# Kernel tuning notes

Measured on AMD Instinct MI355X. Metric: run time of the kernel, lower is better.

Reference implementation:

```python
import jax, jax.numpy as jnp
import numpy as np

SCALE_FACTORS = (1, 2, 4)
N, T, F = 4096, 128, 128
MARKET = 64
MIX = sum(T // k for k in SCALE_FACTORS)  # 224


def hardswish(x):
    return x * jnp.clip(x + 3.0, 0.0, 6.0) * (1.0 / 6.0)


def layernorm2d(x, g, b, eps=1e-5):
    # LayerNorm with normalized_shape == last two dims (as in torch nn.LayerNorm((A, B)))
    mu = jnp.mean(x, axis=(-2, -1), keepdims=True)
    var = jnp.var(x, axis=(-2, -1), keepdims=True)
    return (x - mu) * jax.lax.rsqrt(var + eps) * g + b


def setup_inputs() -> dict:
    key = jax.random.key(0)
    ks = jax.random.split(key, 32)
    inp = {"x": jax.random.normal(ks[0], (N, T, F), jnp.float32)}
    i = 1
    for si, k in enumerate(SCALE_FACTORS):
        tk = T // k
        inp[f"cw{si}"] = jax.random.normal(ks[i], (F, F, k), jnp.float32) * 0.05; i += 1
        inp[f"cb{si}"] = jnp.zeros((F,), jnp.float32)
        inp[f"lg{si}"] = jnp.ones((tk, F), jnp.float32)
        inp[f"lb{si}"] = jnp.zeros((tk, F), jnp.float32)
        inp[f"L1_{si}"] = jax.random.normal(ks[i], (tk, tk), jnp.float32) * 0.01; i += 1
        inp[f"L2_{si}"] = jax.random.normal(ks[i], (tk, tk), jnp.float32) * 0.01; i += 1
    inp["fc_w"] = jax.random.normal(ks[i], (1, F), jnp.float32) * 0.05; i += 1
    inp["fc_b"] = jnp.zeros((1,), jnp.float32)
    inp["sm_lg"] = jnp.ones((N, MIX), jnp.float32)
    inp["sm_lb"] = jnp.zeros((N, MIX), jnp.float32)
    inp["M1"] = jax.random.normal(ks[i], (MARKET, N), jnp.float32); i += 1
    inp["M2"] = jax.random.normal(ks[i], (N, MARKET), jnp.float32); i += 1
    inp["sm_fc_w"] = jax.random.normal(ks[i], (1, 2 * MIX), jnp.float32) * 0.02; i += 1
    inp["sm_fc_b"] = jnp.zeros((1,), jnp.float32)
    return inp


def _forward(x, cw0, cb0, lg0, lb0, L1_0, L2_0,
             cw1, cb1, lg1, lb1, L1_1, L2_1,
             cw2, cb2, lg2, lb2, L1_2, L2_2,
             fc_w, fc_b, sm_lg, sm_lb, M1, M2, sm_fc_w, sm_fc_b):
    n, t, f = x.shape
    per_scale = ((cw0, cb0, lg0, lb0, L1_0, L2_0),
                 (cw1, cb1, lg1, lb1, L1_1, L2_1),
                 (cw2, cb2, lg2, lb2, L1_2, L2_2))
    parts = []
    for k, (cw, cb, lg, lb, L1, L2) in zip(SCALE_FACTORS, per_scale):
        tk = t // k
        # Conv1d(kernel=k, stride=k) == blockwise contraction over non-overlapping windows
        xr = x.transpose(0, 2, 1).reshape(n, f, tk, k)          # (n, F_in, tk, k)
        xt = jnp.einsum('nitk,oik->nto', xr, cw) + cb            # (n, tk, F)
        # TimeMixing: ragged prefix loop == single lower-triangular matmul over time
        mask = jnp.tril(jnp.ones((tk, tk), x.dtype))
        h = layernorm2d(xt, lg, lb)
        u = hardswish(jnp.einsum('ts,nsf->ntf', L1 * mask, h))
        v = jnp.einsum('ts,nsf->ntf', L2 * mask, u)
        xt = xt + v
        parts.append(xt @ fc_w[0] + fc_b[0])                     # (n, tk)
    h = jnp.concatenate(parts, axis=1)                           # (n, MIX)
    # StockMixing
    hn = layernorm2d(h, sm_lg, sm_lb)
    z = M2 @ hardswish(M1 @ hn)                                  # (n, MIX)
    out = jnp.concatenate([h, h + z], axis=1)                    # (n, 2*MIX)
    return out @ sm_fc_w[0][:, None] + sm_fc_b                   # (n, 1)


def reference(x, cw0, cb0, lg0, lb0, L1_0, L2_0,
              cw1, cb1, lg1, lb1, L1_1, L2_1,
              cw2, cb2, lg2, lb2, L1_2, L2_2,
              fc_w, fc_b, sm_lg, sm_lb, M1, M2, sm_fc_w, sm_fc_b):
    return _forward(x, cw0, cb0, lg0, lb0, L1_0, L2_0,
                    cw1, cb1, lg1, lb1, L1_1, L2_1,
                    cw2, cb2, lg2, lb2, L1_2, L2_2,
                    fc_w, fc_b, sm_lg, sm_lb, M1, M2, sm_fc_w, sm_fc_b)
```

## Files before the change

### kernel.cpp

```cpp
#include <hip/hip_runtime.h>
#include <stdint.h>

typedef __attribute__((ext_vector_type(8))) short short8;
typedef __attribute__((ext_vector_type(4))) float f32x4;
typedef __attribute__((ext_vector_type(4))) unsigned short us4;

__device__ __forceinline__ unsigned short f2bf(float f) {
  union { float f; unsigned int i; } v; v.f = f;
  unsigned int r = (v.i + 0x7FFFu + ((v.i >> 16) & 1u)) >> 16;
  return (unsigned short)r;
}
__device__ __forceinline__ float hswish(float x) {
  float t = fminf(fmaxf(x + 3.f, 0.f), 6.f);
  return x * t * (1.f / 6.f);
}

__global__ void prep_kernel(const float* __restrict__ cw0,
                            const float* __restrict__ cw1,
                            const float* __restrict__ cw2,
                            unsigned short* __restrict__ cwLT0,
                            unsigned short* __restrict__ cwLT1,
                            unsigned short* __restrict__ cwLT2) {
  int idx = blockIdx.x * 256 + threadIdx.x;
  if (idx < 16384) {
    cwLT0[idx] = f2bf(cw0[idx]);
  } else if (idx < 16384 + 32768) {
    int t = idx - 16384;
    int o = t >> 8, m = t & 255;
    int j = m >> 7, i = m & 127;
    cwLT1[o * 256 + m] = f2bf(cw1[(o * 128 + i) * 2 + j]);
  } else if (idx < 114688) {
    int t = idx - 49152;
    int o = t >> 9, m = t & 511;
    int j = m >> 7, i = m & 127;
    cwLT2[o * 512 + m] = f2bf(cw2[(o * 128 + i) * 4 + j]);
  }
}

template <int S>
__launch_bounds__(256, 2)
__global__ void s1_kernel(const float* __restrict__ x,
                          const float* __restrict__ cb,
                          const float* __restrict__ lg,
                          const float* __restrict__ lb,
                          const float* __restrict__ L1,
                          const float* __restrict__ L2,
                          const float* __restrict__ fc_w,
                          const float* __restrict__ fc_b,
                          const unsigned short* __restrict__ cwLT,
                          float* __restrict__ h_out) {
  constexpr int K   = 128 << S;
  constexpr int TK  = 128 >> S;
  constexpr int OFF = (S == 0) ? 0 : (S == 1 ? 128 : 192);
  constexpr int nT  = (S == 0) ? 2 : 1;
  constexpr int nO  = (S == 2) ? 4 : 8;
  constexpr int CW  = (TK >= 64) ? 64 : TK;
  constexpr int NCC = K / 64;
  constexpr int NTC = TK / CW;
  constexpr int HTP = TK + 8;
  constexpr int LP  = CW + 8;
  constexpr int R1E = (HTP > 72 ? HTP : 72) * 128;

  extern __shared__ char smem[];
  unsigned short* R0 = (unsigned short*)smem;
  unsigned short* R1 = (unsigned short*)(smem + TK * 72 * 2);
  float* scratch = (float*)(smem + TK * 72 * 2 + R1E * 2);

  const int tid  = threadIdx.x;
  const int wave = tid >> 6;
  const int lane = tid & 63;
  const int quad = lane >> 4;
  const int l16  = lane & 15;
  const int n    = blockIdx.x;
  const float* xn = x + (size_t)n * (128 * 128);

  const int Tbase = (S == 0) ? wave * 2 : ((S == 1) ? wave : (wave & 1));
  const int Obase = (S == 2) ? ((wave >> 1) * 4) : 0;

  if (tid < 128) scratch[tid] = fc_w[tid];
  if (tid < TK) scratch[128 + tid] = 0.f;

  f32x4 acc[nT][nO];
#pragma unroll
  for (int tt = 0; tt < nT; ++tt)
#pragma unroll
    for (int oo = 0; oo < nO; ++oo)
      acc[tt][oo] = (f32x4){0.f, 0.f, 0.f, 0.f};

  for (int c = 0; c < NCC; ++c) {
    for (int i = tid; i < TK * 16; i += 256) {
      int t = i >> 4, c4 = (i & 15) * 4;
      const float4 v = *(const float4*)(xn + t * K + c * 64 + c4);
      us4 p; p[0] = f2bf(v.x); p[1] = f2bf(v.y); p[2] = f2bf(v.z); p[3] = f2bf(v.w);
      *(us4*)&R0[t * 72 + c4] = p;
    }
    for (int i = tid; i < 128 * 16; i += 256) {
      int o = i >> 4, c4 = (i & 15) * 4;
      *(us4*)&R1[o * 72 + c4] = *(const us4*)&cwLT[o * K + c * 64 + c4];
    }
    __syncthreads();
#pragma unroll
    for (int ks = 0; ks < 2; ++ks) {
      short8 a[nT];
#pragma unroll
      for (int tt = 0; tt < nT; ++tt)
        a[tt] = *(const short8*)&R0[((Tbase + tt) * 16 + l16) * 72 + ks * 32 + quad * 8];
#pragma unroll
      for (int oo = 0; oo < nO; ++oo) {
        short8 b = *(const short8*)&R1[((Obase + oo) * 16 + l16) * 72 + ks * 32 + quad * 8];
#pragma unroll
        for (int tt = 0; tt < nT; ++tt)
          acc[tt][oo] = __builtin_amdgcn_mfma_f32_16x16x32_bf16(a[tt], b, acc[tt][oo], 0, 0, 0);
      }
    }
    __syncthreads();
  }

  float sum = 0.f, ss = 0.f;
#pragma unroll
  for (int oo = 0; oo < nO; ++oo) {
    float cbv = cb[(Obase + oo) * 16 + l16];
#pragma unroll
    for (int tt = 0; tt < nT; ++tt)
#pragma unroll
      for (int r = 0; r < 4; ++r) {
        float v = acc[tt][oo][r] + cbv;
        acc[tt][oo][r] = v;
        sum += v; ss += v * v;
      }
  }
#pragma unroll
  for (int m = 32; m >= 1; m >>= 1) {
    sum += __shfl_xor(sum, m);
    ss  += __shfl_xor(ss, m);
  }
  if (lane == 0) { scratch[256 + wave * 2] = sum; scratch[257 + wave * 2] = ss; }
  __syncthreads();
  if (tid == 0) {
    float Sm = 0.f, Ssq = 0.f;
    for (int w = 0; w < 4; ++w) { Sm += scratch[256 + w * 2]; Ssq += scratch[257 + w * 2]; }
    float mu = Sm / (float)(TK * 128);
    float var = Ssq / (float)(TK * 128) - mu * mu;
    scratch[264] = mu;
    scratch[265] = rsqrtf(var + 1e-5f);
  }
  __syncthreads();
  const float mu = scratch[264], rsig = scratch[265];

  unsigned short* HT = R1;
#pragma unroll
  for (int tt = 0; tt < nT; ++tt)
#pragma unroll
    for (int oo = 0; oo < nO; ++oo) {
      int o = (Obase + oo) * 16 + l16;
#pragma unroll
      for (int r = 0; r < 4; ++r) {
        int t = (Tbase + tt) * 16 + quad * 4 + r;
        float hv = (acc[tt][oo][r] - mu) * rsig * lg[t * 128 + o] + lb[t * 128 + o];
        HT[o * HTP + t] = f2bf(hv);
      }
    }

  f32x4 uacc[nT][nO];
#pragma unroll
  for (int tt = 0; tt < nT; ++tt)
#pragma unroll
    for (int oo = 0; oo < nO; ++oo)
      uacc[tt][oo] = (f32x4){0.f, 0.f, 0.f, 0.f};

  for (int c = 0; c < NTC; ++c) {
    for (int i = tid; i < TK * (CW / 4); i += 256) {
      int t = i / (CW / 4), s4 = (i % (CW / 4)) * 4;
      int sg = c * CW + s4;
      const float4 v = *(const float4*)(L1 + t * TK + sg);
      us4 p;
      p[0] = (sg     <= t) ? f2bf(v.x) : (unsigned short)0;
      p[1] = (sg + 1 <= t) ? f2bf(v.y) : (unsigned short)0;
      p[2] = (sg + 2 <= t) ? f2bf(v.z) : (unsigned short)0;
      p[3] = (sg + 3 <= t) ? f2bf(v.w) : (unsigned short)0;
      *(us4*)&R0[t * LP + s4] = p;
    }
    __syncthreads();
#pragma unroll
    for (int ks = 0; ks < CW / 32; ++ks) {
      int k0 = c * CW + ks * 32;
      if (k0 <= (Tbase + nT - 1) * 16 + 15) {
        short8 a[nT];
#pragma unroll
        for (int tt = 0; tt < nT; ++tt)
          a[tt] = *(const short8*)&R0[((Tbase + tt) * 16 + l16) * LP + ks * 32 + quad * 8];
#pragma unroll
        for (int oo = 0; oo < nO; ++oo) {
          short8 b = *(const short8*)&HT[((Obase + oo) * 16 + l16) * HTP + k0 + quad * 8];
#pragma unroll
          for (int tt = 0; tt < nT; ++tt)
            if (k0 <= (Tbase + tt) * 16 + 15)
              uacc[tt][oo] = __builtin_amdgcn_mfma_f32_16x16x32_bf16(a[tt], b, uacc[tt][oo], 0, 0, 0);
        }
      }
      __syncthreads();
    }
  }

#pragma unroll
  for (int tt = 0; tt < nT; ++tt)
#pragma unroll
    for (int oo = 0; oo < nO; ++oo) {
      int f = (Obase + oo) * 16 + l16;
#pragma unroll
      for (int r = 0; r < 4; ++r) {
        int t = (Tbase + tt) * 16 + quad * 4 + r;
        float uv = hswish(uacc[tt][oo][r]);
        HT[f * HTP + t] = f2bf(uv);
      }
    }

  for (int c = 0; c < NTC; ++c) {
    for (int i = tid; i < TK * (CW / 4); i += 256) {
      int t = i / (CW / 4), s4 = (i % (CW / 4)) * 4;
      int sg = c * CW + s4;
      const float4 v = *(const float4*)(L2 + t * TK + sg);
      us4 p;
      p[0] = (sg     <= t) ? f2bf(v.x) : (unsigned short)0;
      p[1] = (sg + 1 <= t) ? f2bf(v.y) : (unsigned short)0;
      p[2] = (sg + 2 <= t) ? f2bf(v.z) : (unsigned short)0;
      p[3] = (sg + 3 <= t) ? f2bf(v.w) : (unsigned short)0;
      *(us4*)&R0[t * LP + s4] = p;
    }
    __syncthreads();
#pragma unroll
    for (int ks = 0; ks < CW / 32; ++ks) {
      int k0 = c * CW + ks * 32;
      if (k0 <= (Tbase + nT - 1) * 16 + 15) {
        short8 a[nT];
#pragma unroll
        for (int tt = 0; tt < nT; ++tt)
          a[tt] = *(const short8*)&R0[((Tbase + tt) * 16 + l16) * LP + ks * 32 + quad * 8];
#pragma unroll
        for (int oo = 0; oo < nO; ++oo) {
          short8 b = *(const short8*)&HT[((Obase + oo) * 16 + l16) * HTP + k0 + quad * 8];
#pragma unroll
          for (int tt = 0; tt < nT; ++tt)
            if (k0 <= (Tbase + tt) * 16 + 15)
              acc[tt][oo] = __builtin_amdgcn_mfma_f32_16x16x32_bf16(a[tt], b, acc[tt][oo], 0, 0, 0);
        }
      }
      __syncthreads();
    }
  }

  float* part = scratch + 128;
#pragma unroll
  for (int tt = 0; tt < nT; ++tt)
#pragma unroll
    for (int r = 0; r < 4; ++r) {
      float v = 0.f;
#pragma unroll
      for (int oo = 0; oo < nO; ++oo)
        v += acc[tt][oo][r] * scratch[(Obase + oo) * 16 + l16];
      v += __shfl_xor(v, 1); v += __shfl_xor(v, 2);
      v += __shfl_xor(v, 4); v += __shfl_xor(v, 8);
      if (l16 == 0) atomicAdd(&part[(Tbase + tt) * 16 + quad * 4 + r], v);
    }
  __syncthreads();
  if (tid < TK) h_out[(size_t)n * 224 + OFF + tid] = part[tid] + fc_b[0];
}

__global__ void stats_kernel(const float* __restrict__ h, float* __restrict__ stats) {
  int base = blockIdx.x * 4096;
  float s = 0.f, ss = 0.f;
  for (int j = 0; j < 16; ++j) {
    float v = h[base + j * 256 + threadIdx.x];
    s += v; ss += v * v;
  }
  int lane = threadIdx.x & 63, wave = threadIdx.x >> 6;
#pragma unroll
  for (int m = 32; m >= 1; m >>= 1) { s += __shfl_xor(s, m); ss += __shfl_xor(ss, m); }
  __shared__ float red[8];
  if (lane == 0) { red[wave * 2] = s; red[wave * 2 + 1] = ss; }
  __syncthreads();
  if (threadIdx.x == 0) {
    atomicAdd(&stats[0], red[0] + red[2] + red[4] + red[6]);
    atomicAdd(&stats[1], red[1] + red[3] + red[5] + red[7]);
  }
}

__global__ void mix1_kernel(const float* __restrict__ h,
                            const float* __restrict__ sm_lg,
                            const float* __restrict__ sm_lb,
                            const float* __restrict__ M1,
                            const float* __restrict__ stats,
                            float* __restrict__ A) {
  const int m = blockIdx.x;
  const int seg = blockIdx.y;
  const int r = threadIdx.x & 63;
  const int ch = threadIdx.x >> 6;
  const float inv = 1.f / 917504.f;
  float mu = stats[0] * inv;
  float var = stats[1] * inv - mu * mu;
  float rsig = rsqrtf(var + 1e-5f);
  float acc = 0.f;
  int n0 = seg * 1024 + ch * 256;
  for (int i = 0; i < 256; ++i) {
    int n = n0 + i;
    float hn = (h[n * 224 + m] - mu) * rsig * sm_lg[n * 224 + m] + sm_lb[n * 224 + m];
    acc += M1[r * 4096 + n] * hn;
  }
  __shared__ float red[256];
  red[threadIdx.x] = acc;
  __syncthreads();
  if (threadIdx.x < 64)
    atomicAdd(&A[threadIdx.x * 224 + m],
              red[threadIdx.x] + red[64 + threadIdx.x] + red[128 + threadIdx.x] + red[192 + threadIdx.x]);
}

__global__ void mix2_kernel(const float* __restrict__ A,
                            const float* __restrict__ sm_fc_w,
                            float* __restrict__ cvec) {
  int r = threadIdx.x & 63, ch = threadIdx.x >> 6;
  float acc = 0.f;
  for (int j = ch; j < 224; j += 4)
    acc += hswish(A[r * 224 + j]) * sm_fc_w[224 + j];
  __shared__ float red[256];
  red[threadIdx.x] = acc;
  __syncthreads();
  if (threadIdx.x < 64)
    cvec[threadIdx.x] = red[threadIdx.x] + red[64 + threadIdx.x] + red[128 + threadIdx.x] + red[192 + threadIdx.x];
}

__global__ void out_kernel(const float* __restrict__ h,
                           const float* __restrict__ M2,
                           const float* __restrict__ cvec,
                           const float* __restrict__ sm_fc_w,
                           const float* __restrict__ sm_fc_b,
                           float* __restrict__ out) {
  int wave = threadIdx.x >> 6, lane = threadIdx.x & 63;
  int n = blockIdx.x * 4 + wave;
  float acc = M2[n * 64 + lane] * cvec[lane];
  for (int j = lane; j < 224; j += 64)
    acc += h[n * 224 + j] * (sm_fc_w[j] + sm_fc_w[224 + j]);
#pragma unroll
  for (int m = 32; m >= 1; m >>= 1) acc += __shfl_xor(acc, m);
  if (lane == 0) out[n] = acc + sm_fc_b[0];
}

extern "C" void kernel_launch(void* const* d_in, const int* in_sizes, int n_in,
                              void* d_out, int out_size, void* d_ws, size_t ws_size,
                              hipStream_t stream) {
  const float* x      = (const float*)d_in[0];
  const float* cw0    = (const float*)d_in[1];
  const float* cb0    = (const float*)d_in[2];
  const float* lg0    = (const float*)d_in[3];
  const float* lb0    = (const float*)d_in[4];
  const float* L1_0   = (const float*)d_in[5];
  const float* L2_0   = (const float*)d_in[6];
  const float* cw1    = (const float*)d_in[7];
  const float* cb1    = (const float*)d_in[8];
  const float* lg1    = (const float*)d_in[9];
  const float* lb1    = (const float*)d_in[10];
  const float* L1_1   = (const float*)d_in[11];
  const float* L2_1   = (const float*)d_in[12];
  const float* cw2    = (const float*)d_in[13];
  const float* cb2    = (const float*)d_in[14];
  const float* lg2    = (const float*)d_in[15];
  const float* lb2    = (const float*)d_in[16];
  const float* L1_2   = (const float*)d_in[17];
  const float* L2_2   = (const float*)d_in[18];
  const float* fc_w   = (const float*)d_in[19];
  const float* fc_b   = (const float*)d_in[20];
  const float* sm_lg  = (const float*)d_in[21];
  const float* sm_lb  = (const float*)d_in[22];
  const float* M1     = (const float*)d_in[23];
  const float* M2     = (const float*)d_in[24];
  const float* sm_fc_w = (const float*)d_in[25];
  const float* sm_fc_b = (const float*)d_in[26];

  char* ws = (char*)d_ws;
  unsigned short* cwLT0 = (unsigned short*)(ws);
  unsigned short* cwLT1 = (unsigned short*)(ws + 32768);
  unsigned short* cwLT2 = (unsigned short*)(ws + 98304);
  float* h     = (float*)(ws + 229376);
  float* stats = (float*)(ws + 3899392);
  float* A     = (float*)(ws + 3899648);
  float* cvec  = (float*)(ws + 3956992);

  prep_kernel<<<448, 256, 0, stream>>>(cw0, cw1, cw2, cwLT0, cwLT1, cwLT2);

  auto smemBytes = [](int S) -> size_t {
    int TK = 128 >> S;
    int HTP = TK + 8;
    int r1 = (HTP > 72 ? HTP : 72) * 128;
    return (size_t)TK * 72 * 2 + (size_t)r1 * 2 + 266 * 4;
  };

  s1_kernel<0><<<4096, 256, smemBytes(0), stream>>>(x, cb0, lg0, lb0, L1_0, L2_0, fc_w, fc_b, cwLT0, h);
  s1_kernel<1><<<4096, 256, smemBytes(1), stream>>>(x, cb1, lg1, lb1, L1_1, L2_1, fc_w, fc_b, cwLT1, h);
  s1_kernel<2><<<4096, 256, smemBytes(2), stream>>>(x, cb2, lg2, lb2, L1_2, L2_2, fc_w, fc_b, cwLT2, h);

  hipMemsetAsync(ws + 3899392, 0, 57600, stream);

  stats_kernel<<<224, 256, 0, stream>>>(h, stats);
  mix1_kernel<<<dim3(224, 4), 256, 0, stream>>>(h, sm_lg, sm_lb, M1, stats, A);
  mix2_kernel<<<1, 256, 0, stream>>>(A, sm_fc_w, cvec);
  out_kernel<<<1024, 256, 0, stream>>>(h, M2, cvec, sm_fc_w, sm_fc_b, (float*)d_out);
}
```

Measured before the change: 894.3 us.

## Fuse three per-scale kernels into one block pass with direct register loads

The three separate scale kernels become one fused kernel that runs all three scale passes per sample, so each x row is read once per block and stays cache-local across scales instead of coming through three launches. The conv GEMM now loads x and the bf16 weights straight from global memory into MFMA registers, dropping LDS staging and its barriers. The masked bf16 L1/L2 conversion moves into the prep kernel instead of being redone in every block. The HT tile uses an XOR-swizzled layout in place of padding to avoid LDS bank conflicts. In exchange, global loads are not coalesced through shared memory, register pressure may rise, and per-block work is serialized across scales.

```diff
diff --git a/kernel.cpp b/kernel.cpp
--- a/kernel.cpp
+++ b/kernel.cpp
@@ -3,123 +3,112 @@
 
 typedef __attribute__((ext_vector_type(8))) short short8;
 typedef __attribute__((ext_vector_type(4))) float f32x4;
-typedef __attribute__((ext_vector_type(4))) unsigned short us4;
 
 __device__ __forceinline__ unsigned short f2bf(float f) {
   union { float f; unsigned int i; } v; v.f = f;
-  unsigned int r = (v.i + 0x7FFFu + ((v.i >> 16) & 1u)) >> 16;
-  return (unsigned short)r;
+  return (unsigned short)((v.i + 0x7FFFu + ((v.i >> 16) & 1u)) >> 16);
 }
 __device__ __forceinline__ float hswish(float x) {
   float t = fminf(fmaxf(x + 3.f, 0.f), 6.f);
   return x * t * (1.f / 6.f);
 }
-
-__global__ void prep_kernel(const float* __restrict__ cw0,
-                            const float* __restrict__ cw1,
+__device__ __forceinline__ short8 ldcvt8(const float* __restrict__ p) {
+  float4 v0 = *(const float4*)p;
+  float4 v1 = *(const float4*)(p + 4);
+  short8 r;
+  r[0] = (short)f2bf(v0.x); r[1] = (short)f2bf(v0.y);
+  r[2] = (short)f2bf(v0.z); r[3] = (short)f2bf(v0.w);
+  r[4] = (short)f2bf(v1.x); r[5] = (short)f2bf(v1.y);
+  r[6] = (short)f2bf(v1.z); r[7] = (short)f2bf(v1.w);
+  return r;
+}
+
+__global__ void prep_kernel(const float* __restrict__ cw0, const float* __restrict__ cw1,
                             const float* __restrict__ cw2,
-                            unsigned short* __restrict__ cwLT0,
-                            unsigned short* __restrict__ cwLT1,
-                            unsigned short* __restrict__ cwLT2) {
+                            const float* __restrict__ L1_0, const float* __restrict__ L2_0,
+                            const float* __restrict__ L1_1, const float* __restrict__ L2_1,
+                            const float* __restrict__ L1_2, const float* __restrict__ L2_2,
+                            unsigned short* __restrict__ ws16) {
   int idx = blockIdx.x * 256 + threadIdx.x;
   if (idx < 16384) {
-    cwLT0[idx] = f2bf(cw0[idx]);
-  } else if (idx < 16384 + 32768) {
-    int t = idx - 16384;
-    int o = t >> 8, m = t & 255;
-    int j = m >> 7, i = m & 127;
-    cwLT1[o * 256 + m] = f2bf(cw1[(o * 128 + i) * 2 + j]);
+    ws16[idx] = f2bf(cw0[idx]);
+  } else if (idx < 49152) {
+    int t = idx - 16384; int o = t >> 8, m = t & 255, j = m >> 7, i = m & 127;
+    ws16[idx] = f2bf(cw1[(o * 128 + i) * 2 + j]);
   } else if (idx < 114688) {
-    int t = idx - 49152;
-    int o = t >> 9, m = t & 511;
-    int j = m >> 7, i = m & 127;
-    cwLT2[o * 512 + m] = f2bf(cw2[(o * 128 + i) * 4 + j]);
+    int t = idx - 49152; int o = t >> 9, m = t & 511, j = m >> 7, i = m & 127;
+    ws16[idx] = f2bf(cw2[(o * 128 + i) * 4 + j]);
+  } else if (idx < 131072) {
+    int u = idx - 114688; int t = u >> 7, s = u & 127;
+    ws16[idx] = (s <= t) ? f2bf(L1_0[u]) : (unsigned short)0;
+  } else if (idx < 147456) {
+    int u = idx - 131072; int t = u >> 7, s = u & 127;
+    ws16[idx] = (s <= t) ? f2bf(L2_0[u]) : (unsigned short)0;
+  } else if (idx < 151552) {
+    int u = idx - 147456; int t = u >> 6, s = u & 63;
+    ws16[idx] = (s <= t) ? f2bf(L1_1[u]) : (unsigned short)0;
+  } else if (idx < 155648) {
+    int u = idx - 151552; int t = u >> 6, s = u & 63;
+    ws16[idx] = (s <= t) ? f2bf(L2_1[u]) : (unsigned short)0;
+  } else if (idx < 156672) {
+    int u = idx - 155648; int t = u >> 5, s = u & 31;
+    ws16[idx] = (s <= t) ? f2bf(L1_2[u]) : (unsigned short)0;
+  } else if (idx < 157696) {
+    int u = idx - 156672; int t = u >> 5, s = u & 31;
+    ws16[idx] = (s <= t) ? f2bf(L2_2[u]) : (unsigned short)0;
   }
 }
 
 template <int S>
-__launch_bounds__(256, 2)
-__global__ void s1_kernel(const float* __restrict__ x,
-                          const float* __restrict__ cb,
-                          const float* __restrict__ lg,
-                          const float* __restrict__ lb,
-                          const float* __restrict__ L1,
-                          const float* __restrict__ L2,
-                          const float* __restrict__ fc_w,
-                          const float* __restrict__ fc_b,
-                          const unsigned short* __restrict__ cwLT,
-                          float* __restrict__ h_out) {
-  constexpr int K   = 128 << S;
-  constexpr int TK  = 128 >> S;
-  constexpr int OFF = (S == 0) ? 0 : (S == 1 ? 128 : 192);
-  constexpr int nT  = (S == 0) ? 2 : 1;
-  constexpr int nO  = (S == 2) ? 4 : 8;
-  constexpr int CW  = (TK >= 64) ? 64 : TK;
-  constexpr int NCC = K / 64;
-  constexpr int NTC = TK / CW;
-  constexpr int HTP = TK + 8;
-  constexpr int LP  = CW + 8;
-  constexpr int R1E = (HTP > 72 ? HTP : 72) * 128;
-
-  extern __shared__ char smem[];
-  unsigned short* R0 = (unsigned short*)smem;
-  unsigned short* R1 = (unsigned short*)(smem + TK * 72 * 2);
-  float* scratch = (float*)(smem + TK * 72 * 2 + R1E * 2);
-
-  const int tid  = threadIdx.x;
-  const int wave = tid >> 6;
-  const int lane = tid & 63;
-  const int quad = lane >> 4;
-  const int l16  = lane & 15;
-  const int n    = blockIdx.x;
-  const float* xn = x + (size_t)n * (128 * 128);
-
-  const int Tbase = (S == 0) ? wave * 2 : ((S == 1) ? wave : (wave & 1));
-  const int Obase = (S == 2) ? ((wave >> 1) * 4) : 0;
-
-  if (tid < 128) scratch[tid] = fc_w[tid];
-  if (tid < TK) scratch[128 + tid] = 0.f;
-
-  f32x4 acc[nT][nO];
-#pragma unroll
-  for (int tt = 0; tt < nT; ++tt)
-#pragma unroll
-    for (int oo = 0; oo < nO; ++oo)
-      acc[tt][oo] = (f32x4){0.f, 0.f, 0.f, 0.f};
-
-  for (int c = 0; c < NCC; ++c) {
-    for (int i = tid; i < TK * 16; i += 256) {
-      int t = i >> 4, c4 = (i & 15) * 4;
-      const float4 v = *(const float4*)(xn + t * K + c * 64 + c4);
-      us4 p; p[0] = f2bf(v.x); p[1] = f2bf(v.y); p[2] = f2bf(v.z); p[3] = f2bf(v.w);
-      *(us4*)&R0[t * 72 + c4] = p;
-    }
-    for (int i = tid; i < 128 * 16; i += 256) {
-      int o = i >> 4, c4 = (i & 15) * 4;
-      *(us4*)&R1[o * 72 + c4] = *(const us4*)&cwLT[o * K + c * 64 + c4];
-    }
-    __syncthreads();
-#pragma unroll
-    for (int ks = 0; ks < 2; ++ks) {
-      short8 a[nT];
+__device__ __forceinline__ void scale_pass(
+    const float* __restrict__ xn,
+    const float* __restrict__ cb, const float* __restrict__ lg, const float* __restrict__ lb,
+    const unsigned short* __restrict__ cwLT,
+    const unsigned short* __restrict__ L1b, const unsigned short* __restrict__ L2b,
+    unsigned short* __restrict__ HT, float* __restrict__ scr, float* __restrict__ part,
+    float* __restrict__ hout, float fcb,
+    int wave, int lane, int quad, int l16, int tid) {
+  constexpr int K  = 128 << S;
+  constexpr int TK = 128 >> S;
+  constexpr int nT = (S == 0) ? 4 : (S == 1) ? 2 : 1;
+  constexpr int NK = K / 32;
+  constexpr int NTK = TK / 32;
+  constexpr int CMASK = TK / 8 - 1;
+
+  const int Tb = (wave & 1) * nT;
+  const int Ob = (wave >> 1) * 4;
+
+  __syncthreads();
+  if (tid < TK) part[tid] = 0.f;
+
+  f32x4 acc[nT][4];
+#pragma unroll
+  for (int tt = 0; tt < nT; ++tt)
+#pragma unroll
+    for (int oo = 0; oo < 4; ++oo) acc[tt][oo] = (f32x4){0.f, 0.f, 0.f, 0.f};
+
+#pragma unroll
+  for (int ks = 0; ks < NK; ++ks) {
+    short8 a[nT];
+#pragma unroll
+    for (int tt = 0; tt < nT; ++tt) {
+      int t = (Tb + tt) * 16 + l16;
+      a[tt] = ldcvt8(xn + t * K + ks * 32 + quad * 8);
+    }
+#pragma unroll
+    for (int oo = 0; oo < 4; ++oo) {
+      int o = (Ob + oo) * 16 + l16;
+      short8 b = *(const short8*)&cwLT[o * K + ks * 32 + quad * 8];
 #pragma unroll
       for (int tt = 0; tt < nT; ++tt)
-        a[tt] = *(const short8*)&R0[((Tbase + tt) * 16 + l16) * 72 + ks * 32 + quad * 8];
-#pragma unroll
-      for (int oo = 0; oo < nO; ++oo) {
-        short8 b = *(const short8*)&R1[((Obase + oo) * 16 + l16) * 72 + ks * 32 + quad * 8];
-#pragma unroll
-        for (int tt = 0; tt < nT; ++tt)
-          acc[tt][oo] = __builtin_amdgcn_mfma_f32_16x16x32_bf16(a[tt], b, acc[tt][oo], 0, 0, 0);
-      }
-    }
-    __syncthreads();
+        acc[tt][oo] = __builtin_amdgcn_mfma_f32_16x16x32_bf16(a[tt], b, acc[tt][oo], 0, 0, 0);
+    }
   }
 
   float sum = 0.f, ss = 0.f;
 #pragma unroll
-  for (int oo = 0; oo < nO; ++oo) {
-    float cbv = cb[(Obase + oo) * 16 + l16];
+  for (int oo = 0; oo < 4; ++oo) {
+    float cbv = cb[(Ob + oo) * 16 + l16];
 #pragma unroll
     for (int tt = 0; tt < nT; ++tt)
 #pragma unroll
@@ -130,140 +119,155 @@
       }
   }
 #pragma unroll
-  for (int m = 32; m >= 1; m >>= 1) {
-    sum += __shfl_xor(sum, m);
-    ss  += __shfl_xor(ss, m);
-  }
-  if (lane == 0) { scratch[256 + wave * 2] = sum; scratch[257 + wave * 2] = ss; }
+  for (int m = 32; m >= 1; m >>= 1) { sum += __shfl_xor(sum, m); ss += __shfl_xor(ss, m); }
+  if (lane == 0) { scr[256 + wave * 2] = sum; scr[257 + wave * 2] = ss; }
   __syncthreads();
   if (tid == 0) {
-    float Sm = 0.f, Ssq = 0.f;
-    for (int w = 0; w < 4; ++w) { Sm += scratch[256 + w * 2]; Ssq += scratch[257 + w * 2]; }
+    float Sm = scr[256] + scr[258] + scr[260] + scr[262];
+    float Sq = scr[257] + scr[259] + scr[261] + scr[263];
     float mu = Sm / (float)(TK * 128);
-    float var = Ssq / (float)(TK * 128) - mu * mu;
-    scratch[264] = mu;
-    scratch[265] = rsqrtf(var + 1e-5f);
-  }
-  __syncthreads();
-  const float mu = scratch[264], rsig = scratch[265];
-
-  unsigned short* HT = R1;
-#pragma unroll
-  for (int tt = 0; tt < nT; ++tt)
-#pragma unroll
-    for (int oo = 0; oo < nO; ++oo) {
-      int o = (Obase + oo) * 16 + l16;
-#pragma unroll
-      for (int r = 0; r < 4; ++r) {
-        int t = (Tbase + tt) * 16 + quad * 4 + r;
-        float hv = (acc[tt][oo][r] - mu) * rsig * lg[t * 128 + o] + lb[t * 128 + o];
-        HT[o * HTP + t] = f2bf(hv);
-      }
-    }
-
-  f32x4 uacc[nT][nO];
-#pragma unroll
-  for (int tt = 0; tt < nT; ++tt)
-#pragma unroll
-    for (int oo = 0; oo < nO; ++oo)
-      uacc[tt][oo] = (f32x4){0.f, 0.f, 0.f, 0.f};
-
-  for (int c = 0; c < NTC; ++c) {
-    for (int i = tid; i < TK * (CW / 4); i += 256) {
-      int t = i / (CW / 4), s4 = (i % (CW / 4)) * 4;
-      int sg = c * CW + s4;
-      const float4 v = *(const float4*)(L1 + t * TK + sg);
-      us4 p;
-      p[0] = (sg     <= t) ? f2bf(v.x) : (unsigned short)0;
-      p[1] = (sg + 1 <= t) ? f2bf(v.y) : (unsigned short)0;
-      p[2] = (sg + 2 <= t) ? f2bf(v.z) : (unsigned short)0;
-      p[3] = (sg + 3 <= t) ? f2bf(v.w) : (unsigned short)0;
-      *(us4*)&R0[t * LP + s4] = p;
-    }
-    __syncthreads();
-#pragma unroll
-    for (int ks = 0; ks < CW / 32; ++ks) {
-      int k0 = c * CW + ks * 32;
-      if (k0 <= (Tbase + nT - 1) * 16 + 15) {
-        short8 a[nT];
-#pragma unroll
-        for (int tt = 0; tt < nT; ++tt)
-          a[tt] = *(const short8*)&R0[((Tbase + tt) * 16 + l16) * LP + ks * 32 + quad * 8];
-#pragma unroll
-        for (int oo = 0; oo < nO; ++oo) {
-          short8 b = *(const short8*)&HT[((Obase + oo) * 16 + l16) * HTP + k0 + quad * 8];
-#pragma unroll
-          for (int tt = 0; tt < nT; ++tt)
-            if (k0 <= (Tbase + tt) * 16 + 15)
-              uacc[tt][oo] = __builtin_amdgcn_mfma_f32_16x16x32_bf16(a[tt], b, uacc[tt][oo], 0, 0, 0);
-        }
-      }
-      __syncthreads();
-    }
-  }
-
-#pragma unroll
-  for (int tt = 0; tt < nT; ++tt)
-#pragma unroll
-    for (int oo = 0; oo < nO; ++oo) {
-      int f = (Obase + oo) * 16 + l16;
-#pragma unroll
-      for (int r = 0; r < 4; ++r) {
-        int t = (Tbase + tt) * 16 + quad * 4 + r;
-        float uv = hswish(uacc[tt][oo][r]);
-        HT[f * HTP + t] = f2bf(uv);
-      }
-    }
-
-  for (int c = 0; c < NTC; ++c) {
-    for (int i = tid; i < TK * (CW / 4); i += 256) {
-      int t = i / (CW / 4), s4 = (i % (CW / 4)) * 4;
-      int sg = c * CW + s4;
-      const float4 v = *(const float4*)(L2 + t * TK + sg);
-      us4 p;
-      p[0] = (sg     <= t) ? f2bf(v.x) : (unsigned short)0;
-      p[1] = (sg + 1 <= t) ? f2bf(v.y) : (unsigned short)0;
-      p[2] = (sg + 2 <= t) ? f2bf(v.z) : (unsigned short)0;
-      p[3] = (sg + 3 <= t) ? f2bf(v.w) : (unsigned short)0;
-      *(us4*)&R0[t * LP + s4] = p;
-    }
-    __syncthreads();
-#pragma unroll
-    for (int ks = 0; ks < CW / 32; ++ks) {
-      int k0 = c * CW + ks * 32;
-      if (k0 <= (Tbase + nT - 1) * 16 + 15) {
-        short8 a[nT];
-#pragma unroll
-        for (int tt = 0; tt < nT; ++tt)
-          a[tt] = *(const short8*)&R0[((Tbase + tt) * 16 + l16) * LP + ks * 32 + quad * 8];
-#pragma unroll
-        for (int oo = 0; oo < nO; ++oo) {
-          short8 b = *(const short8*)&HT[((Obase + oo) * 16 + l16) * HTP + k0 + quad * 8];
-#pragma unroll
-          for (int tt = 0; tt < nT; ++tt)
-            if (k0 <= (Tbase + tt) * 16 + 15)
-              acc[tt][oo] = __builtin_amdgcn_mfma_f32_16x16x32_bf16(a[tt], b, acc[tt][oo], 0, 0, 0);
-        }
-      }
-      __syncthreads();
-    }
-  }
-
-  float* part = scratch + 128;
+    float var = Sq / (float)(TK * 128) - mu * mu;
+    scr[264] = mu; scr[265] = rsqrtf(var + 1e-5f);
+  }
+  __syncthreads();
+  const float mu = scr[264], rsig = scr[265];
+
 #pragma unroll
   for (int tt = 0; tt < nT; ++tt)
 #pragma unroll
     for (int r = 0; r < 4; ++r) {
       float v = 0.f;
 #pragma unroll
-      for (int oo = 0; oo < nO; ++oo)
-        v += acc[tt][oo][r] * scratch[(Obase + oo) * 16 + l16];
+      for (int oo = 0; oo < 4; ++oo) v += acc[tt][oo][r] * scr[(Ob + oo) * 16 + l16];
       v += __shfl_xor(v, 1); v += __shfl_xor(v, 2);
       v += __shfl_xor(v, 4); v += __shfl_xor(v, 8);
-      if (l16 == 0) atomicAdd(&part[(Tbase + tt) * 16 + quad * 4 + r], v);
-    }
-  __syncthreads();
-  if (tid < TK) h_out[(size_t)n * 224 + OFF + tid] = part[tid] + fc_b[0];
+      if (l16 == 0) atomicAdd(&part[(Tb + tt) * 16 + quad * 4 + r], v);
+    }
+
+#pragma unroll
+  for (int tt = 0; tt < nT; ++tt)
+#pragma unroll
+    for (int oo = 0; oo < 4; ++oo) {
+      int f = (Ob + oo) * 16 + l16;
+      int kf = (f ^ (f >> 3)) & CMASK;
+#pragma unroll
+      for (int r = 0; r < 4; ++r) {
+        int t = (Tb + tt) * 16 + quad * 4 + r;
+        float hv = (acc[tt][oo][r] - mu) * rsig * lg[t * 128 + f] + lb[t * 128 + f];
+        HT[f * TK + (((t >> 3) ^ kf) << 3) + (t & 7)] = f2bf(hv);
+      }
+    }
+  __syncthreads();
+
+#pragma unroll
+  for (int tt = 0; tt < nT; ++tt)
+#pragma unroll
+    for (int oo = 0; oo < 4; ++oo) acc[tt][oo] = (f32x4){0.f, 0.f, 0.f, 0.f};
+#pragma unroll
+  for (int ks = 0; ks < NTK; ++ks) {
+    int k0 = ks * 32;
+    if (k0 > (Tb + nT - 1) * 16 + 15) continue;
+    short8 a[nT];
+#pragma unroll
+    for (int tt = 0; tt < nT; ++tt)
+      if (k0 <= (Tb + tt) * 16 + 15) {
+        int t = (Tb + tt) * 16 + l16;
+        a[tt] = *(const short8*)&L1b[t * TK + k0 + quad * 8];
+      }
+#pragma unroll
+    for (int oo = 0; oo < 4; ++oo) {
+      int f = (Ob + oo) * 16 + l16;
+      int kf = (f ^ (f >> 3)) & CMASK;
+      short8 b = *(const short8*)&HT[f * TK + (((ks * 4 + quad) ^ kf) << 3)];
+#pragma unroll
+      for (int tt = 0; tt < nT; ++tt)
+        if (k0 <= (Tb + tt) * 16 + 15)
+          acc[tt][oo] = __builtin_amdgcn_mfma_f32_16x16x32_bf16(a[tt], b, acc[tt][oo], 0, 0, 0);
+    }
+  }
+  __syncthreads();
+
+#pragma unroll
+  for (int tt = 0; tt < nT; ++tt)
+#pragma unroll
+    for (int oo = 0; oo < 4; ++oo) {
+      int f = (Ob + oo) * 16 + l16;
+      int kf = (f ^ (f >> 3)) & CMASK;
+#pragma unroll
+      for (int r = 0; r < 4; ++r) {
+        int t = (Tb + tt) * 16 + quad * 4 + r;
+        HT[f * TK + (((t >> 3) ^ kf) << 3) + (t & 7)] = f2bf(hswish(acc[tt][oo][r]));
+      }
+    }
+  __syncthreads();
+
+#pragma unroll
+  for (int tt = 0; tt < nT; ++tt)
+#pragma unroll
+    for (int oo = 0; oo < 4; ++oo) acc[tt][oo] = (f32x4){0.f, 0.f, 0.f, 0.f};
+#pragma unroll
+  for (int ks = 0; ks < NTK; ++ks) {
+    int k0 = ks * 32;
+    if (k0 > (Tb + nT - 1) * 16 + 15) continue;
+    short8 a[nT];
+#pragma unroll
+    for (int tt = 0; tt < nT; ++tt)
+      if (k0 <= (Tb + tt) * 16 + 15) {
+        int t = (Tb + tt) * 16 + l16;
+        a[tt] = *(const short8*)&L2b[t * TK + k0 + quad * 8];
+      }
+#pragma unroll
+    for (int oo = 0; oo < 4; ++oo) {
+      int f = (Ob + oo) * 16 + l16;
+      int kf = (f ^ (f >> 3)) & CMASK;
+      short8 b = *(const short8*)&HT[f * TK + (((ks * 4 + quad) ^ kf) << 3)];
+#pragma unroll
+      for (int tt = 0; tt < nT; ++tt)
+        if (k0 <= (Tb + tt) * 16 + 15)
+          acc[tt][oo] = __builtin_amdgcn_mfma_f32_16x16x32_bf16(a[tt], b, acc[tt][oo], 0, 0, 0);
+    }
+  }
+
+#pragma unroll
+  for (int tt = 0; tt < nT; ++tt)
+#pragma unroll
+    for (int r = 0; r < 4; ++r) {
+      float v = 0.f;
+#pragma unroll
+      for (int oo = 0; oo < 4; ++oo) v += acc[tt][oo][r] * scr[(Ob + oo) * 16 + l16];
+      v += __shfl_xor(v, 1); v += __shfl_xor(v, 2);
+      v += __shfl_xor(v, 4); v += __shfl_xor(v, 8);
+      if (l16 == 0) atomicAdd(&part[(Tb + tt) * 16 + quad * 4 + r], v);
+    }
+  __syncthreads();
+  if (tid < TK) hout[tid] = part[tid] + fcb;
+}
+
+__launch_bounds__(256, 2)
+__global__ void s1_fused(const float* __restrict__ x,
+                         const float* __restrict__ cb0, const float* __restrict__ lg0, const float* __restrict__ lb0,
+                         const float* __restrict__ cb1, const float* __restrict__ lg1, const float* __restrict__ lb1,
+                         const float* __restrict__ cb2, const float* __restrict__ lg2, const float* __restrict__ lb2,
+                         const float* __restrict__ fc_w, const float* __restrict__ fc_b,
+                         const unsigned short* __restrict__ ws16,
+                         float* __restrict__ h_out) {
+  __shared__ unsigned short HT[128 * 128];
+  __shared__ float scr[268];
+  const int tid = threadIdx.x, wave = tid >> 6, lane = tid & 63;
+  const int quad = lane >> 4, l16 = lane & 15;
+  const int n = blockIdx.x;
+  const float* xn = x + (size_t)n * 16384;
+  if (tid < 128) scr[tid] = fc_w[tid];
+  float* part = scr + 128;
+  const float fcb = fc_b[0];
+  float* hout = h_out + (size_t)n * 224;
+
+  scale_pass<0>(xn, cb0, lg0, lb0, ws16, ws16 + 114688, ws16 + 131072,
+                HT, scr, part, hout, fcb, wave, lane, quad, l16, tid);
+  scale_pass<1>(xn, cb1, lg1, lb1, ws16 + 16384, ws16 + 147456, ws16 + 151552,
+                HT, scr, part, hout + 128, fcb, wave, lane, quad, l16, tid);
+  scale_pass<2>(xn, cb2, lg2, lb2, ws16 + 49152, ws16 + 155648, ws16 + 156672,
+                HT, scr, part, hout + 192, fcb, wave, lane, quad, l16, tid);
 }
 
 __global__ void stats_kernel(const float* __restrict__ h, float* __restrict__ stats) {
@@ -291,10 +295,8 @@
                             const float* __restrict__ M1,
                             const float* __restrict__ stats,
                             float* __restrict__ A) {
-  const int m = blockIdx.x;
-  const int seg = blockIdx.y;
-  const int r = threadIdx.x & 63;
-  const int ch = threadIdx.x >> 6;
+  const int m = blockIdx.x, seg = blockIdx.y;
+  const int r = threadIdx.x & 63, ch = threadIdx.x >> 6;
   const float inv = 1.f / 917504.f;
   float mu = stats[0] * inv;
   float var = stats[1] * inv - mu * mu;
@@ -376,29 +378,18 @@
   const float* sm_fc_b = (const float*)d_in[26];
 
   char* ws = (char*)d_ws;
-  unsigned short* cwLT0 = (unsigned short*)(ws);
-  unsigned short* cwLT1 = (unsigned short*)(ws + 32768);
-  unsigned short* cwLT2 = (unsigned short*)(ws + 98304);
-  float* h     = (float*)(ws + 229376);
-  float* stats = (float*)(ws + 3899392);
-  float* A     = (float*)(ws + 3899648);
-  float* cvec  = (float*)(ws + 3956992);
-
-  prep_kernel<<<448, 256, 0, stream>>>(cw0, cw1, cw2, cwLT0, cwLT1, cwLT2);
-
-  auto smemBytes = [](int S) -> size_t {
-    int TK = 128 >> S;
-    int HTP = TK + 8;
-    int r1 = (HTP > 72 ? HTP : 72) * 128;
-    return (size_t)TK * 72 * 2 + (size_t)r1 * 2 + 266 * 4;
-  };
-
-  s1_kernel<0><<<4096, 256, smemBytes(0), stream>>>(x, cb0, lg0, lb0, L1_0, L2_0, fc_w, fc_b, cwLT0, h);
-  s1_kernel<1><<<4096, 256, smemBytes(1), stream>>>(x, cb1, lg1, lb1, L1_1, L2_1, fc_w, fc_b, cwLT1, h);
-  s1_kernel<2><<<4096, 256, smemBytes(2), stream>>>(x, cb2, lg2, lb2, L1_2, L2_2, fc_w, fc_b, cwLT2, h);
-
-  hipMemsetAsync(ws + 3899392, 0, 57600, stream);
-
+  unsigned short* ws16 = (unsigned short*)ws;
+  float* h     = (float*)(ws + 315392);
+  float* stats = (float*)(ws + 3985408);
+  float* A     = (float*)(ws + 3985664);
+  float* cvec  = (float*)(ws + 4043008);
+
+  prep_kernel<<<616, 256, 0, stream>>>(cw0, cw1, cw2, L1_0, L2_0, L1_1, L2_1, L1_2, L2_2, ws16);
+
+  s1_fused<<<4096, 256, 0, stream>>>(x, cb0, lg0, lb0, cb1, lg1, lb1, cb2, lg2, lb2,
+                                     fc_w, fc_b, ws16, h);
+
+  hipMemsetAsync(ws + 3985408, 0, 57600, stream);
   stats_kernel<<<224, 256, 0, stream>>>(h, stats);
   mix1_kernel<<<dim3(224, 4), 256, 0, stream>>>(h, sm_lg, sm_lb, M1, stats, A);
   mix2_kernel<<<1, 256, 0, stream>>>(A, sm_fc_w, cvec);
```

After: 989.6 us. +10.7%, slower.
